# Kernel optimization log

Measured on AMD Instinct MI355X. Metric: run time of the kernel, lower is better.

## Reference

```python
import jax, jax.numpy as jnp
import numpy as np

NUM_GRAPHS = 32
NODES_PER_GRAPH = 256
N = NUM_GRAPHS * NODES_PER_GRAPH
IN_CH, HID, OUT_CH = 64, 256, 32
K = 20
SPACE, PROP = 3, 2
NEG_SLOPE = 0.01  # F.leaky_relu default
BIG = 1e9         # cross-graph distance mask


def _glorot(key, shape):
    fan_in, fan_out = shape
    lim = (6.0 / (fan_in + fan_out)) ** 0.5
    return jax.random.uniform(key, shape, jnp.float32, -lim, lim)


def setup_inputs() -> dict:
    key = jax.random.key(0)
    ks = jax.random.split(key, 16)
    inp = {
        "x": jax.random.normal(ks[0], (N, IN_CH), jnp.float32),
        "batch": jnp.repeat(jnp.arange(NUM_GRAPHS, dtype=jnp.int32), NODES_PER_GRAPH),
    }
    dims = [(IN_CH, HID), (HID, HID), (HID, OUT_CH)]
    i = 1
    for li, (cin, cout) in enumerate(dims, start=1):
        inp[f"Ws{li}"] = _glorot(ks[i], (cin, SPACE)); i += 1
        inp[f"bs{li}"] = jnp.zeros((SPACE,), jnp.float32)
        inp[f"Wh{li}"] = _glorot(ks[i], (cin, PROP)); i += 1
        inp[f"bh{li}"] = jnp.zeros((PROP,), jnp.float32)
        inp[f"Wo{li}"] = _glorot(ks[i], (cin + PROP, cout)); i += 1
        inp[f"bo{li}"] = jnp.zeros((cout,), jnp.float32)
    return inp


def gravnet_conv(x, mask_add, Ws, bs, Wh, bh, Wo, bo):
    s = x @ Ws + bs                                     # [N,3] learned coords
    h = x @ Wh + bh                                     # [N,2] propagate feats
    s2 = jnp.sum(s * s, axis=1)
    d2 = s2[:, None] + s2[None, :] - 2.0 * (s @ s.T)    # [N,N] squared dists
    d2 = jnp.maximum(d2, 0.0) + mask_add                # block within-graph only
    neg_d2, idx = jax.lax.top_k(-d2, K)                 # kNN (includes self)
    w = jnp.exp(10.0 * neg_d2)                          # exp(-10 * d^2)
    agg = jnp.einsum('nk,nkp->np', w, h[idx])           # aggr='add'
    return jnp.concatenate([agg, x], axis=-1) @ Wo + bo  # lin(cat([out, x]))


def _leaky(h):
    return jnp.where(h >= 0, h, NEG_SLOPE * h)


def reference(x, batch,
              Ws1, bs1, Wh1, bh1, Wo1, bo1,
              Ws2, bs2, Wh2, bh2, Wo2, bo2,
              Ws3, bs3, Wh3, bh3, Wo3, bo3):
    mask_add = jnp.where(batch[:, None] == batch[None, :], 0.0, BIG).astype(x.dtype)
    # dropout p=0.0 -> identity
    h = _leaky(gravnet_conv(x, mask_add, Ws1, bs1, Wh1, bh1, Wo1, bo1))
    h = _leaky(gravnet_conv(h, mask_add, Ws2, bs2, Wh2, bh2, Wo2, bo2))
    out = gravnet_conv(h, mask_add, Ws3, bs3, Wh3, bh3, Wo3, bo3)
    # get_zero_nodes: first node of each contiguous graph segment
    b = jnp.concatenate([jnp.zeros((1,), batch.dtype), batch])
    diff = (b[1:] - b[:-1]).at[0].set(1)
    first_idx = jnp.nonzero(diff != 0, size=NUM_GRAPHS)[0]
    return out[first_idx]
```

## Files before the change

kernel.cpp:

```cpp
#include <hip/hip_runtime.h>
#include <hip/hip_bf16.h>


#define NGRAPH 32
#define GN 256
#define NTOT (NGRAPH*GN)
#define KNN 20
#define CTS 257

typedef __attribute__((ext_vector_type(8))) short bf16x8;
typedef __attribute__((ext_vector_type(4))) float f32x4;

__device__ __forceinline__ ushort f2bf(float x) {
    union { float f; unsigned u; } a; a.f = x;
    unsigned r = a.u + 0x7FFFu + ((a.u >> 16) & 1u);
    return (ushort)(r >> 16);
}
__device__ __forceinline__ float bf2f(ushort h) {
    union { unsigned u; float f; } b; b.u = ((unsigned)h) << 16;
    return b.f;
}
__device__ __forceinline__ bf16x8 ld8(const ushort* p) {
    return *reinterpret_cast<const bf16x8*>(p);
}
__device__ __forceinline__ unsigned pack2(ushort a, ushort b) {
    return (unsigned)a | ((unsigned)b << 16);
}

#define DPP_MIN(v, ctrl, rmask) { \
    unsigned _t = (unsigned)__builtin_amdgcn_update_dpp((int)(v), (int)(v), ctrl, rmask, 0xf, false); \
    (v) = _t < (v) ? _t : (v); }
#define DPP_ADD(v, ctrl, rmask) { \
    float _t = __int_as_float(__builtin_amdgcn_update_dpp(0, __float_as_int(v), ctrl, rmask, 0xf, true)); \
    (v) += _t; }
__device__ __forceinline__ unsigned wave_min_u32(unsigned v) {
    DPP_MIN(v, 0x111, 0xf)
    DPP_MIN(v, 0x112, 0xf)
    DPP_MIN(v, 0x114, 0xf)
    DPP_MIN(v, 0x118, 0xf)
    DPP_MIN(v, 0x142, 0xa)
    DPP_MIN(v, 0x143, 0xc)
    return (unsigned)__builtin_amdgcn_readlane((int)v, 63);
}
__device__ __forceinline__ float wave_sum_f32(float v) {
    DPP_ADD(v, 0x111, 0xf)
    DPP_ADD(v, 0x112, 0xf)
    DPP_ADD(v, 0x114, 0xf)
    DPP_ADD(v, 0x118, 0xf)
    DPP_ADD(v, 0x142, 0xa)
    DPP_ADD(v, 0x143, 0xc)
    return __int_as_float(__builtin_amdgcn_readlane(__float_as_int(v), 63));
}

__device__ __forceinline__ void knn_extract(
    unsigned ua, unsigned ub, unsigned uc, unsigned ud,
    float2 hA, float2 hB, float2 hC, float2 hD,
    int lane, float& out0, float& out1)
{
    float acc0 = 0.f, acc1 = 0.f;
#pragma unroll 1
    for (int it = 0; it < KNN; ++it) {
        unsigned m1 = ua < ub ? ua : ub;
        unsigned m2 = uc < ud ? uc : ud;
        unsigned bv = m1 < m2 ? m1 : m2;
        unsigned gv = wave_min_u32(bv);
        float d2 = __uint_as_float(gv);
        float w = __expf(-10.0f * d2);
        unsigned long long mask = __ballot(bv == gv);
        int wl = __ffsll(mask) - 1;
        if (lane == wl) {
            float h0, h1;
            if (ua == gv)      { h0 = hA.x; h1 = hA.y; ua = 0xFFFFFFFFu; }
            else if (ub == gv) { h0 = hB.x; h1 = hB.y; ub = 0xFFFFFFFFu; }
            else if (uc == gv) { h0 = hC.x; h1 = hC.y; uc = 0xFFFFFFFFu; }
            else               { h0 = hD.x; h1 = hD.y; ud = 0xFFFFFFFFu; }
            acc0 = fmaf(w, h0, acc0);
            acc1 = fmaf(w, h1, acc1);
        }
    }
    out0 = wave_sum_f32(acc0);
    out1 = wave_sum_f32(acc1);
}

__device__ __forceinline__ void knn_rows4(
    const float* sh5, int srow, int orow, int lane, float* __restrict__ aggL)
{
    float sjx[4], sjy[4], sjz[4], s2j[4];
    float2 hs[4];
#pragma unroll
    for (int t = 0; t < 4; ++t) {
        int j = lane + 64 * t;
        float x = sh5[j * 5 + 0], y = sh5[j * 5 + 1], z = sh5[j * 5 + 2];
        sjx[t] = x; sjy[t] = y; sjz[t] = z;
        s2j[t] = x * x + y * y + z * z;
        hs[t] = make_float2(sh5[j * 5 + 3], sh5[j * 5 + 4]);
    }
    unsigned key[4][4];
    float acc0[4], acc1[4];
#pragma unroll
    for (int r = 0; r < 4; ++r) {
        int rl = srow + r;
        float s0 = sh5[rl * 5 + 0], s1v = sh5[rl * 5 + 1], s2v = sh5[rl * 5 + 2];
        float s2row = s0 * s0 + s1v * s1v + s2v * s2v;
#pragma unroll
        for (int t = 0; t < 4; ++t) {
            float dot = s0 * sjx[t] + s1v * sjy[t] + s2v * sjz[t];
            float d2 = s2row + s2j[t] - 2.0f * dot;
            key[r][t] = __float_as_uint(d2 > 0.f ? d2 : 0.f);
        }
        acc0[r] = 0.f; acc1[r] = 0.f;
    }
#pragma unroll 1
    for (int it = 0; it < KNN; ++it) {
        unsigned bv[4], gv[4];
#pragma unroll
        for (int r = 0; r < 4; ++r) {
            unsigned m1 = key[r][0] < key[r][1] ? key[r][0] : key[r][1];
            unsigned m2 = key[r][2] < key[r][3] ? key[r][2] : key[r][3];
            bv[r] = m1 < m2 ? m1 : m2;
            gv[r] = bv[r];
        }
#define KSTAGE(ctrl, rmask) { \
        DPP_MIN(gv[0], ctrl, rmask) DPP_MIN(gv[1], ctrl, rmask) \
        DPP_MIN(gv[2], ctrl, rmask) DPP_MIN(gv[3], ctrl, rmask) }
        KSTAGE(0x111, 0xf) KSTAGE(0x112, 0xf) KSTAGE(0x114, 0xf)
        KSTAGE(0x118, 0xf) KSTAGE(0x142, 0xa) KSTAGE(0x143, 0xc)
#undef KSTAGE
#pragma unroll
        for (int r = 0; r < 4; ++r) {
            unsigned g = (unsigned)__builtin_amdgcn_readlane((int)gv[r], 63);
            float w = __expf(-10.0f * __uint_as_float(g));
            unsigned long long mask = __ballot(bv[r] == g);
            int wl = __ffsll(mask) - 1;
            if (lane == wl) {
                float h0, h1;
                if (key[r][0] == g)      { h0 = hs[0].x; h1 = hs[0].y; key[r][0] = 0xFFFFFFFFu; }
                else if (key[r][1] == g) { h0 = hs[1].x; h1 = hs[1].y; key[r][1] = 0xFFFFFFFFu; }
                else if (key[r][2] == g) { h0 = hs[2].x; h1 = hs[2].y; key[r][2] = 0xFFFFFFFFu; }
                else                     { h0 = hs[3].x; h1 = hs[3].y; key[r][3] = 0xFFFFFFFFu; }
                acc0[r] = fmaf(w, h0, acc0[r]);
                acc1[r] = fmaf(w, h1, acc1[r]);
            }
        }
    }
#define SSTAGE(ctrl, rmask) { \
    DPP_ADD(acc0[0], ctrl, rmask) DPP_ADD(acc1[0], ctrl, rmask) \
    DPP_ADD(acc0[1], ctrl, rmask) DPP_ADD(acc1[1], ctrl, rmask) \
    DPP_ADD(acc0[2], ctrl, rmask) DPP_ADD(acc1[2], ctrl, rmask) \
    DPP_ADD(acc0[3], ctrl, rmask) DPP_ADD(acc1[3], ctrl, rmask) }
    SSTAGE(0x111, 0xf) SSTAGE(0x112, 0xf) SSTAGE(0x114, 0xf)
    SSTAGE(0x118, 0xf) SSTAGE(0x142, 0xa) SSTAGE(0x143, 0xc)
#undef SSTAGE
    if (lane == 63) {
#pragma unroll
        for (int r = 0; r < 4; ++r) {
            aggL[(orow + r) * 2 + 0] = acc0[r];
            aggL[(orow + r) * 2 + 1] = acc1[r];
        }
    }
}

__global__ __launch_bounds__(512) void k2_fused(
    const float* __restrict__ X,
    const float* __restrict__ Ws1, const float* __restrict__ bs1,
    const float* __restrict__ Wh1, const float* __restrict__ bh1,
    const float* __restrict__ Wo1, const float* __restrict__ bo1,
    const float* __restrict__ Ws2, const float* __restrict__ Wh2,
    const float* __restrict__ bs2, const float* __restrict__ bh2,
    const float* __restrict__ Wo2,
    ushort* __restrict__ Wt2hi, ushort* __restrict__ Wt2lo,
    ushort* __restrict__ h1hi, ushort* __restrict__ h1lo,
    float* __restrict__ s2, float* __restrict__ hp2)
{
    const int x = blockIdx.x, tid = threadIdx.x;
    if (x >= 256) {
        int t = (x - 256) * 512 + tid;
        int n = t >> 8, c = t & 255;
        float v = Wo2[(size_t)(2 + c) * 256 + n];
        ushort hi = f2bf(v);
        Wt2hi[n * 256 + c] = hi;
        Wt2lo[n * 256 + c] = f2bf(v - bf2f(hi));
        return;
    }
    __shared__ float sh5[256 * 5];
    __shared__ float aggL[32 * 2];
    __shared__ ushort Ahi[32 * 64];
    __shared__ ushort Alo[32 * 64];
    __shared__ float CT[32 * CTS];
    __shared__ float part[32 * 16 * 5];

    const int lane = tid & 63, wid = tid >> 6;
    const int g = x >> 3, m0 = x * 32, lr0 = (x & 7) * 32;

    bf16x8 bh[2][2], bl[2][2];
    {
        int nb = wid * 32 + (lane & 15);
        int k0 = (lane >> 4) * 8;
#pragma unroll
        for (int kk = 0; kk < 2; ++kk)
#pragma unroll
            for (int ni = 0; ni < 2; ++ni) {
                union { bf16x8 v; ushort u[8]; } H, L;
#pragma unroll
                for (int j = 0; j < 8; ++j) {
                    float v = Wo1[(size_t)(2 + kk * 32 + k0 + j) * 256 + nb + ni * 16];
                    ushort hi = f2bf(v);
                    H.u[j] = hi;
                    L.u[j] = f2bf(v - bf2f(hi));
                }
                bh[kk][ni] = H.v; bl[kk][ni] = L.v;
            }
    }
    if (tid < 256) {
        const float* xr = X + ((size_t)g * GN + tid) * 64;
        float a0 = 0.f, a1 = 0.f, a2 = 0.f, a3 = 0.f, a4 = 0.f;
#pragma unroll 4
        for (int c0 = 0; c0 < 64; c0 += 4) {
            float4 v = *reinterpret_cast<const float4*>(&xr[c0]);
            float xv[4] = {v.x, v.y, v.z, v.w};
#pragma unroll
            for (int j = 0; j < 4; ++j) {
                int c = c0 + j;
                a0 = fmaf(xv[j], Ws1[c * 3 + 0], a0);
                a1 = fmaf(xv[j], Ws1[c * 3 + 1], a1);
                a2 = fmaf(xv[j], Ws1[c * 3 + 2], a2);
                a3 = fmaf(xv[j], Wh1[c * 2 + 0], a3);
                a4 = fmaf(xv[j], Wh1[c * 2 + 1], a4);
            }
        }
        sh5[tid * 5 + 0] = a0 + bs1[0];
        sh5[tid * 5 + 1] = a1 + bs1[1];
        sh5[tid * 5 + 2] = a2 + bs1[2];
        sh5[tid * 5 + 3] = a3 + bh1[0];
        sh5[tid * 5 + 4] = a4 + bh1[1];
    }
    {
        int row = tid >> 4, c4 = (tid & 15) * 4;
        float4 v = *reinterpret_cast<const float4*>(&X[(size_t)(m0 + row) * 64 + c4]);
        int idx = (row * 64 + c4) ^ ((row & 7) << 3);
        ushort4 hi, lo;
        hi.x = f2bf(v.x); lo.x = f2bf(v.x - bf2f(hi.x));
        hi.y = f2bf(v.y); lo.y = f2bf(v.y - bf2f(hi.y));
        hi.z = f2bf(v.z); lo.z = f2bf(v.z - bf2f(hi.z));
        hi.w = f2bf(v.w); lo.w = f2bf(v.w - bf2f(hi.w));
        *reinterpret_cast<ushort4*>(&Ahi[idx]) = hi;
        *reinterpret_cast<ushort4*>(&Alo[idx]) = lo;
    }
    __syncthreads();

    knn_rows4(sh5, lr0 + wid * 4, wid * 4, lane, aggL);

    f32x4 acc[2][2];
#pragma unroll
    for (int mi = 0; mi < 2; ++mi)
#pragma unroll
        for (int ni = 0; ni < 2; ++ni)
            acc[mi][ni] = (f32x4){0.f, 0.f, 0.f, 0.f};
#pragma unroll
    for (int kk = 0; kk < 2; ++kk) {
        int kch = kk * 32 + (lane >> 4) * 8;
        bf16x8 ah[2], al[2];
#pragma unroll
        for (int mi = 0; mi < 2; ++mi) {
            int r = mi * 16 + (lane & 15);
            int idx = (r * 64 + kch) ^ ((r & 7) << 3);
            ah[mi] = ld8(&Ahi[idx]); al[mi] = ld8(&Alo[idx]);
        }
#pragma unroll
        for (int mi = 0; mi < 2; ++mi)
#pragma unroll
            for (int ni = 0; ni < 2; ++ni) {
                acc[mi][ni] = __builtin_amdgcn_mfma_f32_16x16x32_bf16(ah[mi], bh[kk][ni], acc[mi][ni], 0, 0, 0);
                acc[mi][ni] = __builtin_amdgcn_mfma_f32_16x16x32_bf16(ah[mi], bl[kk][ni], acc[mi][ni], 0, 0, 0);
                acc[mi][ni] = __builtin_amdgcn_mfma_f32_16x16x32_bf16(al[mi], bh[kk][ni], acc[mi][ni], 0, 0, 0);
            }
    }
    __syncthreads();

#pragma unroll
    for (int ni = 0; ni < 2; ++ni) {
        int n = wid * 32 + ni * 16 + (lane & 15);
        float w0 = Wo1[n], w1 = Wo1[256 + n], bz = bo1[n];
#pragma unroll
        for (int mi = 0; mi < 2; ++mi) {
            int mb = mi * 16 + ((lane >> 4) << 2);
#pragma unroll
            for (int r = 0; r < 4; ++r) {
                int ml = mb + r;
                float v = acc[mi][ni][r] + fmaf(aggL[ml * 2 + 0], w0, fmaf(aggL[ml * 2 + 1], w1, bz));
                CT[ml * CTS + n] = v >= 0.f ? v : 0.01f * v;
            }
        }
    }
    __syncthreads();

    {
        int row = tid >> 4, cb = (tid & 15) * 16;
        size_t m = (size_t)(m0 + row);
#pragma unroll
        for (int j = 0; j < 2; ++j) {
            int c = cb + j * 8;
            ushort hi[8], lo[8];
#pragma unroll
            for (int t = 0; t < 8; ++t) {
                float v = CT[row * CTS + c + t];
                hi[t] = f2bf(v);
                lo[t] = f2bf(v - bf2f(hi[t]));
            }
            uint4 wh = make_uint4(pack2(hi[0], hi[1]), pack2(hi[2], hi[3]),
                                  pack2(hi[4], hi[5]), pack2(hi[6], hi[7]));
            uint4 wl = make_uint4(pack2(lo[0], lo[1]), pack2(lo[2], lo[3]),
                                  pack2(lo[4], lo[5]), pack2(lo[6], lo[7]));
            *reinterpret_cast<uint4*>(&h1hi[m * 256 + c]) = wh;
            *reinterpret_cast<uint4*>(&h1lo[m * 256 + c]) = wl;
        }
    }
    {
        int row = tid & 31, sub = tid >> 5;
        float p0 = 0.f, p1 = 0.f, p2 = 0.f, p3 = 0.f, p4 = 0.f;
#pragma unroll
        for (int i = 0; i < 16; ++i) {
            int c = sub * 16 + i;
            float v = CT[row * CTS + c];
            p0 = fmaf(v, Ws2[c * 3 + 0], p0);
            p1 = fmaf(v, Ws2[c * 3 + 1], p1);
            p2 = fmaf(v, Ws2[c * 3 + 2], p2);
            p3 = fmaf(v, Wh2[c * 2 + 0], p3);
            p4 = fmaf(v, Wh2[c * 2 + 1], p4);
        }
        float* pp = &part[(row * 16 + sub) * 5];
        pp[0] = p0; pp[1] = p1; pp[2] = p2; pp[3] = p3; pp[4] = p4;
    }
    __syncthreads();
    if (tid < 160) {
        int row = tid / 5, o = tid - row * 5;
        float sum = 0.f;
#pragma unroll
        for (int k = 0; k < 16; ++k) sum += part[(row * 16 + k) * 5 + o];
        if (o < 3) s2[(m0 + row) * 3 + o] = bs2[o] + sum;
        else       hp2[(m0 + row) * 2 + (o - 3)] = bh2[o - 3] + sum;
    }
}

__global__ __launch_bounds__(512) void k3_fused(
    const float* __restrict__ s2, const float* __restrict__ hp2,
    const ushort* __restrict__ h1hi, const ushort* __restrict__ h1lo,
    const ushort* __restrict__ Wt2hi, const ushort* __restrict__ Wt2lo,
    const float* __restrict__ Wo2, const float* __restrict__ bo2,
    const float* __restrict__ Ws3, const float* __restrict__ Wh3,
    const float* __restrict__ bs3, const float* __restrict__ bh3,
    float* __restrict__ h2c, float* __restrict__ s3, float* __restrict__ hp3)
{
    __shared__ float sh5[256 * 5];
    __shared__ float aggL[32 * 2];
    __shared__ float CT[32 * CTS];
    __shared__ float part[32 * 16 * 5];

    const int x = blockIdx.x, tid = threadIdx.x;
    const int lane = tid & 63, wid = tid >> 6;
    const int g = x >> 3, m0 = x * 32, lr0 = (x & 7) * 32;

    if (tid < 256) {
        int node = g * GN + tid;
        sh5[tid * 5 + 0] = s2[node * 3 + 0];
        sh5[tid * 5 + 1] = s2[node * 3 + 1];
        sh5[tid * 5 + 2] = s2[node * 3 + 2];
        sh5[tid * 5 + 3] = hp2[node * 2 + 0];
        sh5[tid * 5 + 4] = hp2[node * 2 + 1];
    }
    __syncthreads();
    knn_rows4(sh5, lr0 + wid * 4, wid * 4, lane, aggL);
    __syncthreads();

    f32x4 acc[2][2];
#pragma unroll
    for (int mi = 0; mi < 2; ++mi)
#pragma unroll
        for (int ni = 0; ni < 2; ++ni)
            acc[mi][ni] = (f32x4){0.f, 0.f, 0.f, 0.f};
#pragma unroll 2
    for (int kof = 0; kof < 256; kof += 32) {
        int kch = kof + (lane >> 4) * 8;
        bf16x8 ah[2], al[2], bh[2], bl[2];
#pragma unroll
        for (int mi = 0; mi < 2; ++mi) {
            size_t off = (size_t)(m0 + mi * 16 + (lane & 15)) * 256 + kch;
            ah[mi] = ld8(h1hi + off); al[mi] = ld8(h1lo + off);
        }
#pragma unroll
        for (int ni = 0; ni < 2; ++ni) {
            size_t off = (size_t)(wid * 32 + ni * 16 + (lane & 15)) * 256 + kch;
            bh[ni] = ld8(Wt2hi + off); bl[ni] = ld8(Wt2lo + off);
        }
#pragma unroll
        for (int mi = 0; mi < 2; ++mi)
#pragma unroll
            for (int ni = 0; ni < 2; ++ni) {
                acc[mi][ni] = __builtin_amdgcn_mfma_f32_16x16x32_bf16(ah[mi], bh[ni], acc[mi][ni], 0, 0, 0);
                acc[mi][ni] = __builtin_amdgcn_mfma_f32_16x16x32_bf16(ah[mi], bl[ni], acc[mi][ni], 0, 0, 0);
                acc[mi][ni] = __builtin_amdgcn_mfma_f32_16x16x32_bf16(al[mi], bh[ni], acc[mi][ni], 0, 0, 0);
            }
    }

#pragma unroll
    for (int ni = 0; ni < 2; ++ni) {
        int n = wid * 32 + ni * 16 + (lane & 15);
        float w0 = Wo2[n], w1 = Wo2[256 + n], bz = bo2[n];
#pragma unroll
        for (int mi = 0; mi < 2; ++mi) {
            int mb = mi * 16 + ((lane >> 4) << 2);
#pragma unroll
            for (int r = 0; r < 4; ++r) {
                int ml = mb + r;
                float v = acc[mi][ni][r] + fmaf(aggL[ml * 2 + 0], w0, fmaf(aggL[ml * 2 + 1], w1, bz));
                CT[ml * CTS + n] = v >= 0.f ? v : 0.01f * v;
            }
        }
    }
    __syncthreads();

    if ((x & 7) == 0 && tid < 256) h2c[g * 256 + tid] = CT[tid];

    {
        int row = tid & 31, sub = tid >> 5;
        float p0 = 0.f, p1 = 0.f, p2 = 0.f, p3 = 0.f, p4 = 0.f;
#pragma unroll
        for (int i = 0; i < 16; ++i) {
            int c = sub * 16 + i;
            float v = CT[row * CTS + c];
            p0 = fmaf(v, Ws3[c * 3 + 0], p0);
            p1 = fmaf(v, Ws3[c * 3 + 1], p1);
            p2 = fmaf(v, Ws3[c * 3 + 2], p2);
            p3 = fmaf(v, Wh3[c * 2 + 0], p3);
            p4 = fmaf(v, Wh3[c * 2 + 1], p4);
        }
        float* pp = &part[(row * 16 + sub) * 5];
        pp[0] = p0; pp[1] = p1; pp[2] = p2; pp[3] = p3; pp[4] = p4;
    }
    __syncthreads();
    if (tid < 160) {
        int row = tid / 5, o = tid - row * 5;
        float sum = 0.f;
#pragma unroll
        for (int k = 0; k < 16; ++k) sum += part[(row * 16 + k) * 5 + o];
        if (o < 3) s3[(m0 + row) * 3 + o] = bs3[o] + sum;
        else       hp3[(m0 + row) * 2 + (o - 3)] = bh3[o - 3] + sum;
    }
}

__global__ __launch_bounds__(256) void knn3_final(
    const float* __restrict__ s, const float* __restrict__ h,
    const float* __restrict__ h2c,
    const float* __restrict__ Wo, const float* __restrict__ bo,
    float* __restrict__ out)
{
    __shared__ float aggL[2];
    __shared__ float pm[8][32];
    int g = blockIdx.x, tid = threadIdx.x;
    if (tid < 64) {
        int lane = tid;
        int base = g * GN, row = g * GN;
        float s0 = s[row * 3 + 0], s1v = s[row * 3 + 1], s2v = s[row * 3 + 2];
        float s2row = s0 * s0 + s1v * s1v + s2v * s2v;
        unsigned key[4]; float2 hs[4];
#pragma unroll
        for (int t = 0; t < 4; ++t) {
            int j = base + lane + 64 * t;
            float xx = s[j * 3 + 0], y = s[j * 3 + 1], z = s[j * 3 + 2];
            float dot = s0 * xx + s1v * y + s2v * z;
            float d2 = s2row + (xx * xx + y * y + z * z) - 2.0f * dot;
            key[t] = __float_as_uint(d2 > 0.f ? d2 : 0.f);
            hs[t] = *reinterpret_cast<const float2*>(&h[(size_t)j * 2]);
        }
        float a0, a1;
        knn_extract(key[0], key[1], key[2], key[3], hs[0], hs[1], hs[2], hs[3], lane, a0, a1);
        if (lane == 63) { aggL[0] = a0; aggL[1] = a1; }
    }
    __syncthreads();
    int o = tid & 31, seg = tid >> 5;
    const float* xr = h2c + g * 256;
    float p = 0.f;
#pragma unroll
    for (int i = 0; i < 32; ++i) {
        int c = seg * 32 + i;
        p = fmaf(xr[c], Wo[(2 + c) * 32 + o], p);
    }
    pm[seg][o] = p;
    __syncthreads();
    if (tid < 32) {
        float acc = fmaf(aggL[0], Wo[o], fmaf(aggL[1], Wo[32 + o], bo[o]));
#pragma unroll
        for (int k = 0; k < 8; ++k) acc += pm[k][o];
        out[g * 32 + o] = acc;
    }
}

extern "C" void kernel_launch(void* const* d_in, const int* in_sizes, int n_in,
                              void* d_out, int out_size, void* d_ws, size_t ws_size,
                              hipStream_t stream) {
    const float* X   = (const float*)d_in[0];
    const float* Ws1 = (const float*)d_in[2];  const float* bs1 = (const float*)d_in[3];
    const float* Wh1 = (const float*)d_in[4];  const float* bh1 = (const float*)d_in[5];
    const float* Wo1 = (const float*)d_in[6];  const float* bo1 = (const float*)d_in[7];
    const float* Ws2 = (const float*)d_in[8];  const float* bs2 = (const float*)d_in[9];
    const float* Wh2 = (const float*)d_in[10]; const float* bh2 = (const float*)d_in[11];
    const float* Wo2 = (const float*)d_in[12]; const float* bo2 = (const float*)d_in[13];
    const float* Ws3 = (const float*)d_in[14]; const float* bs3 = (const float*)d_in[15];
    const float* Wh3 = (const float*)d_in[16]; const float* bh3 = (const float*)d_in[17];
    const float* Wo3 = (const float*)d_in[18]; const float* bo3 = (const float*)d_in[19];

    float* p = (float*)d_ws;
    float* s2   = p; p += NTOT * 3;
    float* hp2  = p; p += NTOT * 2;
    float* s3   = p; p += NTOT * 3;
    float* hp3  = p; p += NTOT * 2;
    float* h2c  = p; p += 32 * 256;
    ushort* q = (ushort*)p;
    ushort* h1hi = q; q += (size_t)NTOT * 256;
    ushort* h1lo = q; q += (size_t)NTOT * 256;
    ushort* Wt2hi = q; q += 256 * 256;
    ushort* Wt2lo = q; q += 256 * 256;

    k2_fused<<<384, 512, 0, stream>>>(X, Ws1, bs1, Wh1, bh1, Wo1, bo1,
                                      Ws2, Wh2, bs2, bh2, Wo2,
                                      Wt2hi, Wt2lo, h1hi, h1lo, s2, hp2);
    k3_fused<<<256, 512, 0, stream>>>(s2, hp2, h1hi, h1lo, Wt2hi, Wt2lo,
                                      Wo2, bo2, Ws3, Wh3, bs3, bh3,
                                      h2c, s3, hp3);
    knn3_final<<<NGRAPH, 256, 0, stream>>>(s3, hp3, h2c, Wo3, bo3, (float*)d_out);
}
```

Measured before the change: 69.37 us.

## Fuse final kNN layer into k3 via last-block-per-graph atomic counter

Removes the separate knn3_final launch. Each k3 block bumps a per-graph atomic counter after writing s3/hp3/h2c, and the eighth block to finish for a graph runs the final kNN and output projection. The counters are zeroed in k2. This saves one kernel launch and its gap in exchange for fences, an atomic per block, and serialized tail work in the last block of each graph.

Result: slower. 78.91 us (+13.8%).

```diff
diff --git a/kernel.cpp b/kernel.cpp
--- a/kernel.cpp
+++ b/kernel.cpp
@@ -170,10 +170,12 @@
     const float* __restrict__ Wo2,
     ushort* __restrict__ Wt2hi, ushort* __restrict__ Wt2lo,
     ushort* __restrict__ h1hi, ushort* __restrict__ h1lo,
-    float* __restrict__ s2, float* __restrict__ hp2)
+    float* __restrict__ s2, float* __restrict__ hp2,
+    unsigned* __restrict__ cnt)
 {
     const int x = blockIdx.x, tid = threadIdx.x;
     if (x >= 256) {
+        if (x == 256 && tid < NGRAPH) cnt[tid] = 0;
         int t = (x - 256) * 512 + tid;
         int n = t >> 8, c = t & 255;
         float v = Wo2[(size_t)(2 + c) * 256 + n];
@@ -349,12 +351,15 @@
     const float* __restrict__ Wo2, const float* __restrict__ bo2,
     const float* __restrict__ Ws3, const float* __restrict__ Wh3,
     const float* __restrict__ bs3, const float* __restrict__ bh3,
-    float* __restrict__ h2c, float* __restrict__ s3, float* __restrict__ hp3)
+    float* __restrict__ h2c, float* __restrict__ s3, float* __restrict__ hp3,
+    const float* __restrict__ Wo3, const float* __restrict__ bo3,
+    unsigned* __restrict__ cnt, float* __restrict__ out)
 {
     __shared__ float sh5[256 * 5];
     __shared__ float aggL[32 * 2];
     __shared__ float CT[32 * CTS];
     __shared__ float part[32 * 16 * 5];
+    __shared__ int lastFlag;
 
     const int x = blockIdx.x, tid = threadIdx.x;
     const int lane = tid & 63, wid = tid >> 6;
@@ -446,52 +451,56 @@
         if (o < 3) s3[(m0 + row) * 3 + o] = bs3[o] + sum;
         else       hp3[(m0 + row) * 2 + (o - 3)] = bh3[o - 3] + sum;
     }
-}
-
-__global__ __launch_bounds__(256) void knn3_final(
-    const float* __restrict__ s, const float* __restrict__ h,
-    const float* __restrict__ h2c,
-    const float* __restrict__ Wo, const float* __restrict__ bo,
-    float* __restrict__ out)
-{
-    __shared__ float aggL[2];
-    __shared__ float pm[8][32];
-    int g = blockIdx.x, tid = threadIdx.x;
+    __syncthreads();
+
+    if (tid == 0) {
+        __threadfence();
+        unsigned old = __hip_atomic_fetch_add(&cnt[g], 1u, __ATOMIC_ACQ_REL,
+                                              __HIP_MEMORY_SCOPE_AGENT);
+        lastFlag = (old == 7);
+        if (lastFlag) __threadfence();
+    }
+    __syncthreads();
+    if (!lastFlag) return;
+
+    float* aggF = aggL;
+    float* pm   = part;
     if (tid < 64) {
-        int lane = tid;
         int base = g * GN, row = g * GN;
-        float s0 = s[row * 3 + 0], s1v = s[row * 3 + 1], s2v = s[row * 3 + 2];
+        float s0 = s3[row * 3 + 0], s1v = s3[row * 3 + 1], s2v = s3[row * 3 + 2];
         float s2row = s0 * s0 + s1v * s1v + s2v * s2v;
         unsigned key[4]; float2 hs[4];
 #pragma unroll
         for (int t = 0; t < 4; ++t) {
-            int j = base + lane + 64 * t;
-            float xx = s[j * 3 + 0], y = s[j * 3 + 1], z = s[j * 3 + 2];
+            int j = base + tid + 64 * t;
+            float xx = s3[j * 3 + 0], y = s3[j * 3 + 1], z = s3[j * 3 + 2];
             float dot = s0 * xx + s1v * y + s2v * z;
             float d2 = s2row + (xx * xx + y * y + z * z) - 2.0f * dot;
             key[t] = __float_as_uint(d2 > 0.f ? d2 : 0.f);
-            hs[t] = *reinterpret_cast<const float2*>(&h[(size_t)j * 2]);
+            hs[t] = *reinterpret_cast<const float2*>(&hp3[(size_t)j * 2]);
         }
         float a0, a1;
-        knn_extract(key[0], key[1], key[2], key[3], hs[0], hs[1], hs[2], hs[3], lane, a0, a1);
-        if (lane == 63) { aggL[0] = a0; aggL[1] = a1; }
-    }
-    __syncthreads();
-    int o = tid & 31, seg = tid >> 5;
-    const float* xr = h2c + g * 256;
-    float p = 0.f;
-#pragma unroll
-    for (int i = 0; i < 32; ++i) {
-        int c = seg * 32 + i;
-        p = fmaf(xr[c], Wo[(2 + c) * 32 + o], p);
-    }
-    pm[seg][o] = p;
+        knn_extract(key[0], key[1], key[2], key[3], hs[0], hs[1], hs[2], hs[3], tid, a0, a1);
+        if (tid == 63) { aggF[0] = a0; aggF[1] = a1; }
+    }
+    __syncthreads();
+    if (tid < 256) {
+        int o = tid & 31, seg = tid >> 5;
+        const float* xr = h2c + g * 256;
+        float p = 0.f;
+#pragma unroll
+        for (int i = 0; i < 32; ++i) {
+            int c = seg * 32 + i;
+            p = fmaf(xr[c], Wo3[(2 + c) * 32 + o], p);
+        }
+        pm[seg * 32 + o] = p;
+    }
     __syncthreads();
     if (tid < 32) {
-        float acc = fmaf(aggL[0], Wo[o], fmaf(aggL[1], Wo[32 + o], bo[o]));
-#pragma unroll
-        for (int k = 0; k < 8; ++k) acc += pm[k][o];
-        out[g * 32 + o] = acc;
+        float accf = fmaf(aggF[0], Wo3[tid], fmaf(aggF[1], Wo3[32 + tid], bo3[tid]));
+#pragma unroll
+        for (int k = 0; k < 8; ++k) accf += pm[k * 32 + tid];
+        out[g * 32 + tid] = accf;
     }
 }
 
@@ -515,6 +524,7 @@
     float* s3   = p; p += NTOT * 3;
     float* hp3  = p; p += NTOT * 2;
     float* h2c  = p; p += 32 * 256;
+    unsigned* cnt = (unsigned*)p; p += 64;
     ushort* q = (ushort*)p;
     ushort* h1hi = q; q += (size_t)NTOT * 256;
     ushort* h1lo = q; q += (size_t)NTOT * 256;
@@ -523,9 +533,8 @@
 
     k2_fused<<<384, 512, 0, stream>>>(X, Ws1, bs1, Wh1, bh1, Wo1, bo1,
                                       Ws2, Wh2, bs2, bh2, Wo2,
-                                      Wt2hi, Wt2lo, h1hi, h1lo, s2, hp2);
+                                      Wt2hi, Wt2lo, h1hi, h1lo, s2, hp2, cnt);
     k3_fused<<<256, 512, 0, stream>>>(s2, hp2, h1hi, h1lo, Wt2hi, Wt2lo,
                                       Wo2, bo2, Ws3, Wh3, bs3, bh3,
-                                      h2c, s3, hp3);
-    knn3_final<<<NGRAPH, 256, 0, stream>>>(s3, hp3, h2c, Wo3, bo3, (float*)d_out);
-}
+                                      h2c, s3, hp3, Wo3, bo3, cnt, (float*)d_out);
+}
```
